# Optimization experiments

Measured on AMD Instinct MI355X. Metric: run time of the kernel, lower is better.

Reference implementation:

```python
import jax, jax.numpy as jnp
import numpy as np

D_MODEL = 1024
N_HEADS = 16
HEAD_DIM = D_MODEL // N_HEADS
WINDOW = 128
NEG = -1e9


def setup_inputs() -> dict:
    key = jax.random.key(0)
    ks = jax.random.split(key, 9)
    s = 1.0 / np.sqrt(D_MODEL)
    x = jax.random.normal(ks[0], (1, 4096, D_MODEL), dtype=jnp.float32)
    Wq = jax.random.uniform(ks[1], (D_MODEL, D_MODEL), jnp.float32, -s, s)
    bq = jax.random.uniform(ks[2], (D_MODEL,), jnp.float32, -s, s)
    Wk = jax.random.uniform(ks[3], (D_MODEL, D_MODEL), jnp.float32, -s, s)
    bk = jax.random.uniform(ks[4], (D_MODEL,), jnp.float32, -s, s)
    Wv = jax.random.uniform(ks[5], (D_MODEL, D_MODEL), jnp.float32, -s, s)
    bv = jax.random.uniform(ks[6], (D_MODEL,), jnp.float32, -s, s)
    Wo = jax.random.uniform(ks[7], (D_MODEL, D_MODEL), jnp.float32, -s, s)
    bo = jax.random.uniform(ks[8], (D_MODEL,), jnp.float32, -s, s)
    return {"x": x, "Wq": Wq, "bq": bq, "Wk": Wk, "bk": bk,
            "Wv": Wv, "bv": bv, "Wo": Wo, "bo": bo}


def reference(x, Wq, bq, Wk, bk, Wv, bv, Wo, bo):
    B, S, _ = x.shape
    scale = 1.0 / np.sqrt(HEAD_DIM)

    def heads(W, b):
        # [B,S,D] -> [B,H,S,hd]  (torch Linear: x @ W.T + b)
        return (x @ W.T + b).reshape(B, S, N_HEADS, HEAD_DIM).transpose(0, 2, 1, 3)

    q = heads(Wq, bq)
    k = heads(Wk, bk)
    v = heads(Wv, bv)

    scores = jnp.einsum('bhqd,bhkd->bhqk', q, k) * scale  # [B,H,S,S]
    i = jnp.arange(S)
    window_mask = jnp.abs(i[:, None] - i[None, :]) <= (WINDOW // 2)  # [S,S]
    scores = jnp.where(window_mask[None, None], scores, NEG)
    attn = jax.nn.softmax(scores, axis=-1)
    ctx = jnp.einsum('bhqk,bhkd->bhqd', attn, v)
    ctx = ctx.transpose(0, 2, 1, 3).reshape(B, S, D_MODEL)
    return ctx @ Wo.T + bo
```

## Files before the change

kernel.cpp:

```cpp
#include <hip/hip_runtime.h>

typedef __bf16 bf16;
typedef __bf16 bf16x8 __attribute__((ext_vector_type(8)));
typedef float floatx4 __attribute__((ext_vector_type(4)));

#define SEQ 4096
#define DM 1024
#define NH 16
#define HD 64
#define SD 3072

__device__ __forceinline__ bf16x8 load8(const bf16* p) {
    return *(const bf16x8*)p;
}

__device__ __forceinline__ void async_ld16(const bf16* g, bf16* l) {
    __builtin_amdgcn_global_load_lds(
        (const __attribute__((address_space(1))) unsigned int*)g,
        (__attribute__((address_space(3))) unsigned int*)l,
        16, 0, 0);
}

__global__ __launch_bounds__(256) void cast_f32_bf16_kernel(
    const float* __restrict__ src, bf16* __restrict__ dst, int n8)
{
    int i = blockIdx.x * blockDim.x + threadIdx.x;
    if (i >= n8) return;
    const float4* s = (const float4*)src;
    float4 a = s[2 * i], b = s[2 * i + 1];
    bf16x8 o;
    o[0] = (bf16)a.x; o[1] = (bf16)a.y; o[2] = (bf16)a.z; o[3] = (bf16)a.w;
    o[4] = (bf16)b.x; o[5] = (bf16)b.y; o[6] = (bf16)b.z; o[7] = (bf16)b.w;
    *(bf16x8*)(dst + 8 * i) = o;
}

__global__ __launch_bounds__(256) void bias_concat_kernel(
    const float* __restrict__ b0, const float* __restrict__ b1,
    const float* __restrict__ b2, float* __restrict__ dst)
{
    int i = blockIdx.x * blockDim.x + threadIdx.x;
    if (i >= 3 * DM) return;
    dst[i] = i < DM ? b0[i] : (i < 2 * DM ? b1[i - DM] : b2[i - 2 * DM]);
}

template <int BM, typename TOUT>
__global__ __launch_bounds__(256) void gemm_lds_kernel(
    const bf16* __restrict__ A,
    const bf16* __restrict__ B,
    const float* __restrict__ bias,
    TOUT* __restrict__ C,
    int M, int N, int K)
{
    constexpr int MI = BM / 32;
    __shared__ bf16 As[BM * 32];
    __shared__ bf16 Bs[128 * 32];

    const int tid  = threadIdx.x;
    const int wave = tid >> 6;
    const int lane = tid & 63;
    const int l15  = lane & 15;
    const int quad = lane >> 4;
    const int m0 = blockIdx.x * BM;
    const int n0 = blockIdx.y * 128;

    const int wm = (wave & 1) * (BM / 2);
    const int wn = (wave >> 1) * 64;

    const int lrow = lane >> 2;
    const int lcol = (lane & 3) * 8;

    const bf16* aptr[2]; bf16* alds[2]; int na = 0;
#pragma unroll
    for (int c = wave; c < BM / 16; c += 4) {
        aptr[na] = A + (size_t)(m0 + c * 16 + lrow) * K + lcol;
        alds[na] = As + c * 512;
        ++na;
    }
    const bf16* bptr[2]; bf16* blds[2];
    {
        int i = 0;
#pragma unroll
        for (int c = wave; c < 8; c += 4) {
            bptr[i] = B + (size_t)(n0 + c * 16 + lrow) * K + lcol;
            blds[i] = Bs + c * 512;
            ++i;
        }
    }

    floatx4 acc[MI][4] = {};

    for (int k0 = 0; k0 < K; k0 += 32) {
        __syncthreads();
#pragma unroll
        for (int i = 0; i < 2; ++i)
            if (i < na) async_ld16(aptr[i] + k0, alds[i]);
#pragma unroll
        for (int i = 0; i < 2; ++i)
            async_ld16(bptr[i] + k0, blds[i]);
        __syncthreads();

        bf16x8 af[MI], bfr[4];
#pragma unroll
        for (int i = 0; i < MI; ++i)
            af[i] = load8(As + (wm + i * 16 + l15) * 32 + quad * 8);
#pragma unroll
        for (int j = 0; j < 4; ++j)
            bfr[j] = load8(Bs + (wn + j * 16 + l15) * 32 + quad * 8);
#pragma unroll
        for (int i = 0; i < MI; ++i)
#pragma unroll
            for (int j = 0; j < 4; ++j)
                acc[i][j] = __builtin_amdgcn_mfma_f32_16x16x32_bf16(af[i], bfr[j], acc[i][j], 0, 0, 0);
    }

#pragma unroll
    for (int j = 0; j < 4; ++j) {
        int n = n0 + wn + j * 16 + l15;
        float bv = bias[n];
#pragma unroll
        for (int i = 0; i < MI; ++i) {
#pragma unroll
            for (int r = 0; r < 4; ++r) {
                int m = m0 + wm + i * 16 + quad * 4 + r;
                C[(size_t)m * N + n] = (TOUT)(acc[i][j][r] + bv);
            }
        }
    }
}

__global__ __launch_bounds__(64) void swattn_kernel(
    const bf16* __restrict__ QKV,
    bf16* __restrict__ ctx)
{
    __shared__ bf16 Plds[16][40];
    __shared__ bf16 Vt[64][40];

    const int lane = threadIdx.x;
    const int l15  = lane & 15;
    const int quad = lane >> 4;
    const int q0   = blockIdx.x * 16;
    const int h    = blockIdx.y;
    const int hoff = h * HD;

    const bf16* qbase = QKV + (size_t)(q0 + l15) * SD + hoff + quad * 8;
    bf16x8 aq0 = load8(qbase);
    bf16x8 aq1 = load8(qbase + 32);

    float mrow[4] = {-INFINITY, -INFINITY, -INFINITY, -INFINITY};
    float lrow[4] = {0.f, 0.f, 0.f, 0.f};
    floatx4 o[4] = {};

    for (int kb = q0 - 64; kb <= q0 + 64; kb += 32) {
        __syncthreads();

#pragma unroll
        for (int it = 0; it < 4; ++it) {
            int krow = it * 8 + (lane >> 3);
            int kg = kb + krow;
            kg = kg < 0 ? 0 : (kg > SEQ - 1 ? SEQ - 1 : kg);
            int d0 = (lane & 7) * 8;
            bf16x8 vv = load8(QKV + (size_t)kg * SD + 2048 + hoff + d0);
#pragma unroll
            for (int j = 0; j < 8; ++j)
                Vt[d0 + j][krow] = vv[j];
        }

        floatx4 sa[2];
#pragma unroll
        for (int nt = 0; nt < 2; ++nt) {
            int key = kb + nt * 16 + l15;
            int kc = key < 0 ? 0 : (key > SEQ - 1 ? SEQ - 1 : key);
            const bf16* kr = QKV + (size_t)kc * SD + 1024 + hoff + quad * 8;
            bf16x8 b0 = load8(kr);
            bf16x8 b1 = load8(kr + 32);
            floatx4 acc = {};
            acc = __builtin_amdgcn_mfma_f32_16x16x32_bf16(aq0, b0, acc, 0, 0, 0);
            acc = __builtin_amdgcn_mfma_f32_16x16x32_bf16(aq1, b1, acc, 0, 0, 0);
            sa[nt] = acc;
        }

#pragma unroll
        for (int r = 0; r < 4; ++r) {
            int q = q0 + quad * 4 + r;
            int k0i = kb + l15;
            int k1i = kb + 16 + l15;
            float v0 = sa[0][r] * 0.125f;
            float v1 = sa[1][r] * 0.125f;
            int d0 = q - k0i, d1 = q - k1i;
            if (d0 > 64 || d0 < -64 || k0i < 0 || k0i >= SEQ) v0 = -1e9f;
            if (d1 > 64 || d1 < -64 || k1i < 0 || k1i >= SEQ) v1 = -1e9f;

            float mx = fmaxf(v0, v1);
            mx = fmaxf(mx, __shfl_xor(mx, 1));
            mx = fmaxf(mx, __shfl_xor(mx, 2));
            mx = fmaxf(mx, __shfl_xor(mx, 4));
            mx = fmaxf(mx, __shfl_xor(mx, 8));
            float mnew = fmaxf(mrow[r], mx);
            float alpha = __expf(mrow[r] - mnew);
            float p0 = __expf(v0 - mnew);
            float p1 = __expf(v1 - mnew);
            float rs = p0 + p1;
            rs += __shfl_xor(rs, 1);
            rs += __shfl_xor(rs, 2);
            rs += __shfl_xor(rs, 4);
            rs += __shfl_xor(rs, 8);
            lrow[r] = lrow[r] * alpha + rs;
            mrow[r] = mnew;
#pragma unroll
            for (int t = 0; t < 4; ++t) o[t][r] *= alpha;
            Plds[quad * 4 + r][l15]      = (bf16)p0;
            Plds[quad * 4 + r][16 + l15] = (bf16)p1;
        }

        __syncthreads();

        bf16x8 ap = load8(&Plds[l15][quad * 8]);
#pragma unroll
        for (int t = 0; t < 4; ++t) {
            bf16x8 bv = load8(&Vt[t * 16 + l15][quad * 8]);
            o[t] = __builtin_amdgcn_mfma_f32_16x16x32_bf16(ap, bv, o[t], 0, 0, 0);
        }
    }

#pragma unroll
    for (int t = 0; t < 4; ++t) {
#pragma unroll
        for (int r = 0; r < 4; ++r) {
            int q = q0 + quad * 4 + r;
            ctx[(size_t)q * DM + hoff + t * 16 + l15] = (bf16)(o[t][r] / lrow[r]);
        }
    }
}

extern "C" void kernel_launch(void* const* d_in, const int* in_sizes, int n_in,
                              void* d_out, int out_size, void* d_ws, size_t ws_size,
                              hipStream_t stream) {
    const float* x  = (const float*)d_in[0];
    const float* Wq = (const float*)d_in[1];
    const float* bq = (const float*)d_in[2];
    const float* Wk = (const float*)d_in[3];
    const float* bk = (const float*)d_in[4];
    const float* Wv = (const float*)d_in[5];
    const float* bv = (const float*)d_in[6];
    const float* Wo = (const float*)d_in[7];
    const float* bo = (const float*)d_in[8];
    float* out = (float*)d_out;

    const size_t XN = (size_t)SEQ * DM;
    const size_t WN = (size_t)DM * DM;

    bf16* xb   = (bf16*)d_ws;
    bf16* Wcat = xb + XN;
    bf16* Wob  = Wcat + 3 * WN;
    bf16* QKV  = Wob + WN;
    bf16* ctx  = QKV + 3 * XN;
    float* bcat = (float*)(ctx + XN);

    int n8 = (int)(XN / 8);
    int w8 = (int)(WN / 8);
    cast_f32_bf16_kernel<<<(n8 + 255) / 256, 256, 0, stream>>>(x, xb, n8);
    cast_f32_bf16_kernel<<<(w8 + 255) / 256, 256, 0, stream>>>(Wq, Wcat, w8);
    cast_f32_bf16_kernel<<<(w8 + 255) / 256, 256, 0, stream>>>(Wk, Wcat + WN, w8);
    cast_f32_bf16_kernel<<<(w8 + 255) / 256, 256, 0, stream>>>(Wv, Wcat + 2 * WN, w8);
    cast_f32_bf16_kernel<<<(w8 + 255) / 256, 256, 0, stream>>>(Wo, Wob, w8);
    bias_concat_kernel<<<(3 * DM + 255) / 256, 256, 0, stream>>>(bq, bk, bv, bcat);

    gemm_lds_kernel<128, bf16><<<dim3(SEQ / 128, SD / 128), 256, 0, stream>>>(
        xb, Wcat, bcat, QKV, SEQ, SD, DM);

    swattn_kernel<<<dim3(SEQ / 16, NH), 64, 0, stream>>>(QKV, ctx);

    gemm_lds_kernel<64, float><<<dim3(SEQ / 64, DM / 128), 256, 0, stream>>>(
        ctx, Wob, bo, out, SEQ, DM, DM);
}
```

Before: 188.9 us.

## Fuse prep casts, vectorize GEMM epilogue, restructure sliding-window attention per block

Merges the five cast launches and the bias concat into one prep kernel, so there are fewer launches. Swaps the MFMA operand order in the GEMM so each lane holds four consecutive columns, which allows vectorized bias loads and 4-wide stores. Rewrites the attention kernel to handle 64 queries per 256-thread block: V for the whole window is loaded and transposed into LDS once, all 9 score tiles are computed, and a single-pass softmax replaces the online one. This cuts repeated K/V loads and per-step barriers, at the cost of more registers and LDS per block.

```diff
diff --git a/kernel.cpp b/kernel.cpp
--- a/kernel.cpp
+++ b/kernel.cpp
@@ -2,6 +2,7 @@
 
 typedef __bf16 bf16;
 typedef __bf16 bf16x8 __attribute__((ext_vector_type(8)));
+typedef __bf16 bf16x4 __attribute__((ext_vector_type(4)));
 typedef float floatx4 __attribute__((ext_vector_type(4)));
 
 #define SEQ 4096
@@ -10,6 +11,10 @@
 #define HD 64
 #define SD 3072
 
+__device__ __forceinline__ floatx4 mfma32(bf16x8 a, bf16x8 b, floatx4 c) {
+    return __builtin_amdgcn_mfma_f32_16x16x32_bf16(a, b, c, 0, 0, 0);
+}
+
 __device__ __forceinline__ bf16x8 load8(const bf16* p) {
     return *(const bf16x8*)p;
 }
@@ -21,26 +26,34 @@
         16, 0, 0);
 }
 
-__global__ __launch_bounds__(256) void cast_f32_bf16_kernel(
-    const float* __restrict__ src, bf16* __restrict__ dst, int n8)
+__global__ __launch_bounds__(256) void prep_kernel(
+    const float* __restrict__ x,  const float* __restrict__ Wq,
+    const float* __restrict__ Wk, const float* __restrict__ Wv,
+    const float* __restrict__ Wo, const float* __restrict__ bq,
+    const float* __restrict__ bk, const float* __restrict__ bv,
+    bf16* __restrict__ xb, bf16* __restrict__ Wcat,
+    bf16* __restrict__ Wob, float* __restrict__ bcat)
 {
-    int i = blockIdx.x * blockDim.x + threadIdx.x;
-    if (i >= n8) return;
-    const float4* s = (const float4*)src;
-    float4 a = s[2 * i], b = s[2 * i + 1];
+    const int WN8 = 131072;
+    const int XN8 = 524288;
+    int b = blockIdx.x;
+    if (b == 4096) {
+        for (int k = threadIdx.x; k < 3 * DM; k += 256)
+            bcat[k] = k < DM ? bq[k] : (k < 2 * DM ? bk[k - DM] : bv[k - 2 * DM]);
+        return;
+    }
+    int c = b * 256 + threadIdx.x;
+    const float* src; bf16* dst;
+    if (c < XN8)              { src = x;  dst = xb; }
+    else if (c < XN8 + WN8)   { src = Wq; dst = Wcat;                 c -= XN8; }
+    else if (c < XN8 + 2*WN8) { src = Wk; dst = Wcat + (size_t)DM*DM;     c -= XN8 + WN8; }
+    else if (c < XN8 + 3*WN8) { src = Wv; dst = Wcat + (size_t)2*DM*DM;   c -= XN8 + 2*WN8; }
+    else                      { src = Wo; dst = Wob;                  c -= XN8 + 3*WN8; }
+    float4 a = ((const float4*)src)[2 * c], d2 = ((const float4*)src)[2 * c + 1];
     bf16x8 o;
-    o[0] = (bf16)a.x; o[1] = (bf16)a.y; o[2] = (bf16)a.z; o[3] = (bf16)a.w;
-    o[4] = (bf16)b.x; o[5] = (bf16)b.y; o[6] = (bf16)b.z; o[7] = (bf16)b.w;
-    *(bf16x8*)(dst + 8 * i) = o;
-}
-
-__global__ __launch_bounds__(256) void bias_concat_kernel(
-    const float* __restrict__ b0, const float* __restrict__ b1,
-    const float* __restrict__ b2, float* __restrict__ dst)
-{
-    int i = blockIdx.x * blockDim.x + threadIdx.x;
-    if (i >= 3 * DM) return;
-    dst[i] = i < DM ? b0[i] : (i < 2 * DM ? b1[i - DM] : b2[i - 2 * DM]);
+    o[0] = (bf16)a.x;  o[1] = (bf16)a.y;  o[2] = (bf16)a.z;  o[3] = (bf16)a.w;
+    o[4] = (bf16)d2.x; o[5] = (bf16)d2.y; o[6] = (bf16)d2.z; o[7] = (bf16)d2.w;
+    *(bf16x8*)(dst + 8 * (size_t)c) = o;
 }
 
 template <int BM, typename TOUT>
@@ -110,125 +123,143 @@
         for (int i = 0; i < MI; ++i)
 #pragma unroll
             for (int j = 0; j < 4; ++j)
-                acc[i][j] = __builtin_amdgcn_mfma_f32_16x16x32_bf16(af[i], bfr[j], acc[i][j], 0, 0, 0);
-    }
-
-#pragma unroll
-    for (int j = 0; j < 4; ++j) {
-        int n = n0 + wn + j * 16 + l15;
-        float bv = bias[n];
-#pragma unroll
-        for (int i = 0; i < MI; ++i) {
-#pragma unroll
-            for (int r = 0; r < 4; ++r) {
-                int m = m0 + wm + i * 16 + quad * 4 + r;
-                C[(size_t)m * N + n] = (TOUT)(acc[i][j][r] + bv);
+                acc[i][j] = mfma32(bfr[j], af[i], acc[i][j]);
+    }
+
+#pragma unroll
+    for (int i = 0; i < MI; ++i) {
+        int xm = m0 + wm + i * 16 + l15;
+#pragma unroll
+        for (int j = 0; j < 4; ++j) {
+            int cn = n0 + wn + j * 16 + quad * 4;
+            float4 bv = *(const float4*)(bias + cn);
+            float v0 = acc[i][j][0] + bv.x;
+            float v1 = acc[i][j][1] + bv.y;
+            float v2 = acc[i][j][2] + bv.z;
+            float v3 = acc[i][j][3] + bv.w;
+            if constexpr (sizeof(TOUT) == 2) {
+                bf16x4 o = {(bf16)v0, (bf16)v1, (bf16)v2, (bf16)v3};
+                *(bf16x4*)((bf16*)C + (size_t)xm * N + cn) = o;
+            } else {
+                float4 o = {v0, v1, v2, v3};
+                *(float4*)((float*)C + (size_t)xm * N + cn) = o;
             }
         }
     }
 }
 
-__global__ __launch_bounds__(64) void swattn_kernel(
+__global__ __launch_bounds__(256, 4) void swattn_kernel(
     const bf16* __restrict__ QKV,
     bf16* __restrict__ ctx)
 {
-    __shared__ bf16 Plds[16][40];
-    __shared__ bf16 Vt[64][40];
-
-    const int lane = threadIdx.x;
+    __shared__ bf16 Vt[64][216];
+    __shared__ bf16 Pc[4][16][40];
+    __shared__ float lred[4][16];
+
+    const int tid  = threadIdx.x;
+    const int wave = tid >> 6;
+    const int lane = tid & 63;
     const int l15  = lane & 15;
     const int quad = lane >> 4;
-    const int q0   = blockIdx.x * 16;
+    const int q0   = blockIdx.x * 64;
     const int h    = blockIdx.y;
     const int hoff = h * HD;
-
-    const bf16* qbase = QKV + (size_t)(q0 + l15) * SD + hoff + quad * 8;
-    bf16x8 aq0 = load8(qbase);
-    bf16x8 aq1 = load8(qbase + 32);
-
-    float mrow[4] = {-INFINITY, -INFINITY, -INFINITY, -INFINITY};
-    float lrow[4] = {0.f, 0.f, 0.f, 0.f};
-    floatx4 o[4] = {};
-
-    for (int kb = q0 - 64; kb <= q0 + 64; kb += 32) {
-        __syncthreads();
-
-#pragma unroll
-        for (int it = 0; it < 4; ++it) {
-            int krow = it * 8 + (lane >> 3);
-            int kg = kb + krow;
-            kg = kg < 0 ? 0 : (kg > SEQ - 1 ? SEQ - 1 : kg);
-            int d0 = (lane & 7) * 8;
-            bf16x8 vv = load8(QKV + (size_t)kg * SD + 2048 + hoff + d0);
-#pragma unroll
-            for (int j = 0; j < 8; ++j)
-                Vt[d0 + j][krow] = vv[j];
-        }
-
-        floatx4 sa[2];
-#pragma unroll
-        for (int nt = 0; nt < 2; ++nt) {
-            int key = kb + nt * 16 + l15;
-            int kc = key < 0 ? 0 : (key > SEQ - 1 ? SEQ - 1 : key);
-            const bf16* kr = QKV + (size_t)kc * SD + 1024 + hoff + quad * 8;
-            bf16x8 b0 = load8(kr);
-            bf16x8 b1 = load8(kr + 32);
-            floatx4 acc = {};
-            acc = __builtin_amdgcn_mfma_f32_16x16x32_bf16(aq0, b0, acc, 0, 0, 0);
-            acc = __builtin_amdgcn_mfma_f32_16x16x32_bf16(aq1, b1, acc, 0, 0, 0);
-            sa[nt] = acc;
-        }
-
+    const int kbase = q0 - 64;
+
+    for (int task = tid; task < 432; task += 256) {
+        int kg = task % 54, dc = task / 54;
+        bf16x8 r[4];
+#pragma unroll
+        for (int i = 0; i < 4; ++i) {
+            int gk = kbase + 4 * kg + i;
+            gk = gk < 0 ? 0 : (gk > SEQ - 1 ? SEQ - 1 : gk);
+            r[i] = load8(QKV + (size_t)gk * SD + 2048 + hoff + dc * 8);
+        }
+#pragma unroll
+        for (int j = 0; j < 8; ++j) {
+            bf16x4 w = { r[0][j], r[1][j], r[2][j], r[3][j] };
+            *(bf16x4*)&Vt[dc * 8 + j][4 * kg] = w;
+        }
+    }
+
+    const int qrow = q0 + wave * 16 + l15;
+    const bf16* qb = QKV + (size_t)qrow * SD + hoff + quad * 8;
+    bf16x8 aq0 = load8(qb), aq1 = load8(qb + 32);
+
+    const int ws = kbase + wave * 16;
+    floatx4 s[9];
+#pragma unroll
+    for (int st = 0; st < 9; ++st) {
+        int kr = ws + st * 16 + l15;
+        int kc2 = kr < 0 ? 0 : (kr > SEQ - 1 ? SEQ - 1 : kr);
+        const bf16* kp = QKV + (size_t)kc2 * SD + 1024 + hoff + quad * 8;
+        bf16x8 b0 = load8(kp), b1 = load8(kp + 32);
+        floatx4 acc = {};
+        acc = mfma32(aq0, b0, acc);
+        acc = mfma32(aq1, b1, acc);
+        s[st] = acc;
+    }
+
+#pragma unroll
+    for (int r = 0; r < 4; ++r) {
+        int row = quad * 4 + r;
+        float mx = -INFINITY;
+#pragma unroll
+        for (int st = 0; st < 9; ++st) {
+            int j = st * 16 + l15;
+            int gk = ws + j;
+            bool ok = (j >= row) && (j <= 128 + row) && (gk >= 0) && (gk < SEQ);
+            float v = ok ? s[st][r] * 0.125f : -1e30f;
+            s[st][r] = v;
+            mx = fmaxf(mx, v);
+        }
+        mx = fmaxf(mx, __shfl_xor(mx, 1));
+        mx = fmaxf(mx, __shfl_xor(mx, 2));
+        mx = fmaxf(mx, __shfl_xor(mx, 4));
+        mx = fmaxf(mx, __shfl_xor(mx, 8));
+        float sum = 0.f;
+#pragma unroll
+        for (int st = 0; st < 9; ++st) {
+            float p = __expf(s[st][r] - mx);
+            s[st][r] = p;
+            sum += p;
+        }
+        sum += __shfl_xor(sum, 1);
+        sum += __shfl_xor(sum, 2);
+        sum += __shfl_xor(sum, 4);
+        sum += __shfl_xor(sum, 8);
+        lred[wave][row] = sum;
+    }
+
+    __syncthreads();
+
+    floatx4 ot[4] = {};
+#pragma unroll
+    for (int kc = 0; kc < 5; ++kc) {
 #pragma unroll
         for (int r = 0; r < 4; ++r) {
-            int q = q0 + quad * 4 + r;
-            int k0i = kb + l15;
-            int k1i = kb + 16 + l15;
-            float v0 = sa[0][r] * 0.125f;
-            float v1 = sa[1][r] * 0.125f;
-            int d0 = q - k0i, d1 = q - k1i;
-            if (d0 > 64 || d0 < -64 || k0i < 0 || k0i >= SEQ) v0 = -1e9f;
-            if (d1 > 64 || d1 < -64 || k1i < 0 || k1i >= SEQ) v1 = -1e9f;
-
-            float mx = fmaxf(v0, v1);
-            mx = fmaxf(mx, __shfl_xor(mx, 1));
-            mx = fmaxf(mx, __shfl_xor(mx, 2));
-            mx = fmaxf(mx, __shfl_xor(mx, 4));
-            mx = fmaxf(mx, __shfl_xor(mx, 8));
-            float mnew = fmaxf(mrow[r], mx);
-            float alpha = __expf(mrow[r] - mnew);
-            float p0 = __expf(v0 - mnew);
-            float p1 = __expf(v1 - mnew);
-            float rs = p0 + p1;
-            rs += __shfl_xor(rs, 1);
-            rs += __shfl_xor(rs, 2);
-            rs += __shfl_xor(rs, 4);
-            rs += __shfl_xor(rs, 8);
-            lrow[r] = lrow[r] * alpha + rs;
-            mrow[r] = mnew;
-#pragma unroll
-            for (int t = 0; t < 4; ++t) o[t][r] *= alpha;
-            Plds[quad * 4 + r][l15]      = (bf16)p0;
-            Plds[quad * 4 + r][16 + l15] = (bf16)p1;
-        }
-
-        __syncthreads();
-
-        bf16x8 ap = load8(&Plds[l15][quad * 8]);
-#pragma unroll
-        for (int t = 0; t < 4; ++t) {
-            bf16x8 bv = load8(&Vt[t * 16 + l15][quad * 8]);
-            o[t] = __builtin_amdgcn_mfma_f32_16x16x32_bf16(ap, bv, o[t], 0, 0, 0);
-        }
-    }
-
-#pragma unroll
-    for (int t = 0; t < 4; ++t) {
-#pragma unroll
-        for (int r = 0; r < 4; ++r) {
-            int q = q0 + quad * 4 + r;
-            ctx[(size_t)q * DM + hoff + t * 16 + l15] = (bf16)(o[t][r] / lrow[r]);
-        }
+            int row = quad * 4 + r;
+            Pc[wave][row][l15] = (bf16)s[2 * kc][r];
+            if (kc < 4)
+                Pc[wave][row][16 + l15] = (bf16)s[2 * kc + 1][r];
+            else
+                Pc[wave][row][16 + l15] = (bf16)0.f;
+        }
+        bf16x8 pb = load8(&Pc[wave][l15][quad * 8]);
+#pragma unroll
+        for (int dt = 0; dt < 4; ++dt) {
+            bf16x8 va = load8(&Vt[dt * 16 + l15][wave * 16 + kc * 32 + quad * 8]);
+            ot[dt] = mfma32(va, pb, ot[dt]);
+        }
+    }
+
+    float linv = 1.0f / lred[wave][l15];
+#pragma unroll
+    for (int dt = 0; dt < 4; ++dt) {
+        bf16x4 o4;
+#pragma unroll
+        for (int r = 0; r < 4; ++r) o4[r] = (bf16)(ot[dt][r] * linv);
+        *(bf16x4*)(ctx + (size_t)qrow * DM + hoff + dt * 16 + quad * 4) = o4;
     }
 }
 
@@ -256,19 +287,13 @@
     bf16* ctx  = QKV + 3 * XN;
     float* bcat = (float*)(ctx + XN);
 
-    int n8 = (int)(XN / 8);
-    int w8 = (int)(WN / 8);
-    cast_f32_bf16_kernel<<<(n8 + 255) / 256, 256, 0, stream>>>(x, xb, n8);
-    cast_f32_bf16_kernel<<<(w8 + 255) / 256, 256, 0, stream>>>(Wq, Wcat, w8);
-    cast_f32_bf16_kernel<<<(w8 + 255) / 256, 256, 0, stream>>>(Wk, Wcat + WN, w8);
-    cast_f32_bf16_kernel<<<(w8 + 255) / 256, 256, 0, stream>>>(Wv, Wcat + 2 * WN, w8);
-    cast_f32_bf16_kernel<<<(w8 + 255) / 256, 256, 0, stream>>>(Wo, Wob, w8);
-    bias_concat_kernel<<<(3 * DM + 255) / 256, 256, 0, stream>>>(bq, bk, bv, bcat);
+    prep_kernel<<<4097, 256, 0, stream>>>(x, Wq, Wk, Wv, Wo, bq, bk, bv,
+                                          xb, Wcat, Wob, bcat);
 
     gemm_lds_kernel<128, bf16><<<dim3(SEQ / 128, SD / 128), 256, 0, stream>>>(
         xb, Wcat, bcat, QKV, SEQ, SD, DM);
 
-    swattn_kernel<<<dim3(SEQ / 16, NH), 64, 0, stream>>>(QKV, ctx);
+    swattn_kernel<<<dim3(SEQ / 64, NH), 256, 0, stream>>>(QKV, ctx);
 
     gemm_lds_kernel<64, float><<<dim3(SEQ / 64, DM / 128), 256, 0, stream>>>(
         ctx, Wob, bo, out, SEQ, DM, DM);
```

New measurement: 186.0 us. About the same (-1.5%).
